# Optimization experiments

Hardware: AMD Instinct MI355X
Metric: run time of the kernel (lower is better)

## Reference

```python
import jax, jax.numpy as jnp
import numpy as np

D_MODEL = 256
N_HEADS = 8
HEAD_DIM = D_MODEL // N_HEADS  # 32
N_LEVELS = 4
N_POINTS = 4
LEVEL_SHAPES = [(100, 100), (50, 50), (25, 25), (13, 13)]
LEVEL_STARTS = [0] + list(np.cumsum([h * w for h, w in LEVEL_SHAPES]))[:-1]
LEN_IN = int(sum(h * w for h, w in LEVEL_SHAPES))  # 13294
BATCH = 2
LEN_Q = LEN_IN  # encoder self-attention


def _offset_bias():
    # faithful to MSDeformAttn._reset_parameters for sampling_offsets bias
    thetas = np.arange(N_HEADS, dtype=np.float32) * (2.0 * np.pi / N_HEADS)
    grid = np.stack([np.cos(thetas), np.sin(thetas)], -1)
    grid = grid / np.abs(grid).max(-1, keepdims=True)
    grid = np.tile(grid.reshape(N_HEADS, 1, 1, 2), (1, N_LEVELS, N_POINTS, 1))
    for i in range(N_POINTS):
        grid[:, :, i, :] *= i + 1
    return jnp.asarray(grid.reshape(-1), dtype=jnp.float32)


def setup_inputs() -> dict:
    key = jax.random.key(0)
    ks = jax.random.split(key, 10)
    s = 1.0 / np.sqrt(D_MODEL)
    inp = {
        "query": jax.random.normal(ks[0], (BATCH, LEN_Q, D_MODEL), jnp.float32),
        "reference_points": jax.random.uniform(ks[1], (BATCH, LEN_Q, N_LEVELS, 2), jnp.float32),
        "input_flatten": jax.random.normal(ks[2], (BATCH, LEN_IN, D_MODEL), jnp.float32),
        "input_spatial_shapes": jnp.asarray(LEVEL_SHAPES, dtype=jnp.int32),
        "W_value": jax.random.normal(ks[3], (D_MODEL, D_MODEL), jnp.float32) * s,
        "b_value": jnp.zeros((D_MODEL,), jnp.float32),
        "W_off": jax.random.normal(ks[4], (D_MODEL, N_HEADS * N_LEVELS * N_POINTS * 2), jnp.float32) * 0.01,
        "b_off": _offset_bias(),
        "W_attn": jax.random.normal(ks[5], (D_MODEL, N_HEADS * N_LEVELS * N_POINTS), jnp.float32) * 0.01,
        "b_attn": jnp.zeros((N_HEADS * N_LEVELS * N_POINTS,), jnp.float32),
        "W_out": jax.random.normal(ks[6], (D_MODEL, D_MODEL), jnp.float32) * s,
        "b_out": jnp.zeros((D_MODEL,), jnp.float32),
    }
    return inp


def _corner(v_t, ix, iy, h, w):
    # v_t: (n, M, h*w, D); ix/iy: (n, M, LqP) int32. Zero padding outside.
    valid = (ix >= 0) & (ix < w) & (iy >= 0) & (iy < h)
    idx = jnp.clip(iy, 0, h - 1) * w + jnp.clip(ix, 0, w - 1)
    g = jnp.take_along_axis(v_t, idx[..., None], axis=2)  # (n, M, LqP, D)
    return g * valid[..., None].astype(v_t.dtype)


def _ms_deform_attn(query, reference_points, input_flatten,
                    W_value, b_value, W_off, b_off, W_attn, b_attn, W_out, b_out):
    n, lq, _ = query.shape
    value = (input_flatten @ W_value + b_value).reshape(n, LEN_IN, N_HEADS, HEAD_DIM)
    offs = (query @ W_off + b_off).reshape(n, lq, N_HEADS, N_LEVELS, N_POINTS, 2)
    aw = jax.nn.softmax(
        (query @ W_attn + b_attn).reshape(n, lq, N_HEADS, N_LEVELS * N_POINTS), axis=-1
    ).reshape(n, lq, N_HEADS, N_LEVELS, N_POINTS)
    # offset_normalizer = (w, h) per level
    norm = jnp.asarray([[w, h] for h, w in LEVEL_SHAPES], dtype=query.dtype)
    loc = reference_points[:, :, None, :, None, :] + offs / norm[None, None, None, :, None, :]

    acc = jnp.zeros((n, N_HEADS, lq, HEAD_DIM), dtype=value.dtype)
    for l, (h, w) in enumerate(LEVEL_SHAPES):
        s0 = LEVEL_STARTS[l]
        v_t = jnp.transpose(value[:, s0:s0 + h * w], (0, 2, 1, 3))  # (n, M, hw, D)
        ll = loc[:, :, :, l]  # (n, lq, M, P, 2) in [0,1]
        # grid_sample bilinear, align_corners=False: pixel = coord*size - 0.5
        x = ll[..., 0] * w - 0.5
        y = ll[..., 1] * h - 0.5
        x0 = jnp.floor(x); y0 = jnp.floor(y)
        tx = x - x0; ty = y - y0
        ix0 = x0.astype(jnp.int32); iy0 = y0.astype(jnp.int32)
        flat = lambda a: jnp.transpose(a, (0, 2, 1, 3)).reshape(n, N_HEADS, lq * N_POINTS)
        ix0f, iy0f = flat(ix0), flat(iy0)
        txf = flat(tx)[..., None]; tyf = flat(ty)[..., None]
        g00 = _corner(v_t, ix0f, iy0f, h, w)
        g01 = _corner(v_t, ix0f + 1, iy0f, h, w)
        g10 = _corner(v_t, ix0f, iy0f + 1, h, w)
        g11 = _corner(v_t, ix0f + 1, iy0f + 1, h, w)
        samp = (g00 * (1 - txf) * (1 - tyf) + g01 * txf * (1 - tyf)
                + g10 * (1 - txf) * tyf + g11 * txf * tyf)
        samp = samp.reshape(n, N_HEADS, lq, N_POINTS, HEAD_DIM)
        wl = jnp.transpose(aw[:, :, :, l], (0, 2, 1, 3))[..., None]  # (n, M, lq, P, 1)
        acc = acc + (samp * wl).sum(axis=3)

    out = jnp.transpose(acc, (0, 2, 1, 3)).reshape(n, lq, D_MODEL)
    return out @ W_out + b_out


def reference(query, reference_points, input_flatten, input_spatial_shapes,
              W_value, b_value, W_off, b_off, W_attn, b_attn, W_out, b_out):
    # input_spatial_shapes carried for signature fidelity; level geometry is static.
    return _ms_deform_attn(query, reference_points, input_flatten,
                           W_value, b_value, W_off, b_off, W_attn, b_attn, W_out, b_out)
```

## Files before the change

### kernel.cpp

```cpp
#include <hip/hip_runtime.h>

#define NH 8
#define HD 32
#define NL 4
#define NP 4
#define DM 256
#define LEN_IN_C 13294
#define LQ_C 13294
#define B_C 2
#define M_TOTAL (B_C * LQ_C)
#define MT_TILES 1662

typedef __attribute__((ext_vector_type(8))) short short8;
typedef __attribute__((ext_vector_type(4))) float floatx4;

__device__ __forceinline__ unsigned short f2bf(float x) {
    union { float f; unsigned int u; } a; a.f = x;
    unsigned int r = (a.u + 0x7FFFu + ((a.u >> 16) & 1u)) >> 16;
    return (unsigned short)r;
}
__device__ __forceinline__ float bflo(unsigned int u) {
    union { unsigned int u; float f; } a; a.u = u << 16; return a.f;
}
__device__ __forceinline__ float bfhi(unsigned int u) {
    union { unsigned int u; float f; } a; a.u = u & 0xffff0000u; return a.f;
}

__global__ __launch_bounds__(256) void conv_a_kernel(const float* __restrict__ A0,
                                                     unsigned short* __restrict__ D0,
                                                     const float* __restrict__ A1,
                                                     unsigned short* __restrict__ D1,
                                                     int M) {
    const float* A = blockIdx.y ? A1 : A0;
    unsigned short* Asw = blockIdx.y ? D1 : D0;
    const int u = blockIdx.x * 256 + threadIdx.x;
    const int lane = u & 63;
    const int kc = (u >> 6) & 7;
    const int rt = u >> 9;
    const int row = rt * 16 + (lane & 15);
    const int col0 = kc * 32 + (lane >> 4) * 8;
    unsigned short tmp[8];
    if (row < M) {
        const float4 f0 = *(const float4*)(A + (size_t)row * 256 + col0);
        const float4 f1 = *(const float4*)(A + (size_t)row * 256 + col0 + 4);
        tmp[0] = f2bf(f0.x); tmp[1] = f2bf(f0.y); tmp[2] = f2bf(f0.z); tmp[3] = f2bf(f0.w);
        tmp[4] = f2bf(f1.x); tmp[5] = f2bf(f1.y); tmp[6] = f2bf(f1.z); tmp[7] = f2bf(f1.w);
    } else {
#pragma unroll
        for (int j = 0; j < 8; ++j) tmp[j] = 0;
    }
    short8 v;
#pragma unroll
    for (int j = 0; j < 8; ++j) v[j] = (short)tmp[j];
    ((short8*)Asw)[u] = v;
}

__device__ __forceinline__ void conv_b_body(const float* __restrict__ W,
                                            unsigned short* __restrict__ Bsw,
                                            int Nsrc, int NTsrc, int NTtotal, int ntOff,
                                            int vblk) {
    const int u = vblk * 256 + threadIdx.x;
    const int lane = u & 63;
    const int unit = u >> 6;
    const int ntl = unit % NTsrc;
    const int kc = unit / NTsrc;
    const int n = ntl * 16 + (lane & 15);
    const int k0 = kc * 32 + (lane >> 4) * 8;
    short8 v;
#pragma unroll
    for (int j = 0; j < 8; ++j)
        v[j] = (short)f2bf(W[(size_t)(k0 + j) * Nsrc + n]);
    ((short8*)Bsw)[(size_t)(kc * NTtotal + ntOff + ntl) * 64 + lane] = v;
}

__global__ __launch_bounds__(256) void conv_weights_kernel(const float* __restrict__ Wv,
                                                           const float* __restrict__ Woff,
                                                           const float* __restrict__ Wattn,
                                                           const float* __restrict__ Wout,
                                                           const float* __restrict__ boff,
                                                           const float* __restrict__ battn,
                                                           unsigned short* __restrict__ BswV,
                                                           unsigned short* __restrict__ BswOA,
                                                           unsigned short* __restrict__ BswO,
                                                           float* __restrict__ fbias) {
    const int blk = blockIdx.x;
    if (blk < 32)        conv_b_body(Wv,    BswV,  256, 16, 16, 0,  blk);
    else if (blk < 64)   conv_b_body(Woff,  BswOA, 256, 16, 24, 0,  blk - 32);
    else if (blk < 80)   conv_b_body(Wattn, BswOA, 128,  8, 24, 16, blk - 64);
    else if (blk < 112)  conv_b_body(Wout,  BswO,  256, 16, 16, 0,  blk - 80);
    else {
        const int t = (blk - 112) * 256 + threadIdx.x;
        if (t < 384) fbias[t] = (t < 256) ? boff[t] : battn[t - 256];
    }
}

template <int NT, bool OUT_BF16>
__global__ __launch_bounds__(256) void mfma_gemm_kernel(const unsigned short* __restrict__ Asw,
                                                        const unsigned short* __restrict__ Bsw,
                                                        const float* __restrict__ bias,
                                                        void* __restrict__ Cout, int M) {
    constexpr int NTW = NT / 4;
    const int tid = threadIdx.x;
    const int lane = tid & 63;
    const int wave = tid >> 6;
    const int rt0 = blockIdx.x * 2;

    const short8* Au = (const short8*)Asw;
    const short8* Bu = (const short8*)Bsw;

    floatx4 acc[2][NTW];
#pragma unroll
    for (int r = 0; r < 2; ++r)
#pragma unroll
        for (int t = 0; t < NTW; ++t) acc[r][t] = (floatx4){0.f, 0.f, 0.f, 0.f};

#pragma unroll 2
    for (int kc = 0; kc < 8; ++kc) {
        const short8 a0 = Au[(size_t)(rt0 * 8 + kc) * 64 + lane];
        const short8 a1 = Au[(size_t)((rt0 + 1) * 8 + kc) * 64 + lane];
#pragma unroll
        for (int t = 0; t < NTW; ++t) {
            const short8 b = Bu[(size_t)(kc * NT + wave * NTW + t) * 64 + lane];
            acc[0][t] = __builtin_amdgcn_mfma_f32_16x16x32_bf16(a0, b, acc[0][t], 0, 0, 0);
            acc[1][t] = __builtin_amdgcn_mfma_f32_16x16x32_bf16(a1, b, acc[1][t], 0, 0, 0);
        }
    }

    const int N = NT * 16;
    const int colq = lane & 15;
    const int rowq = (lane >> 4) * 4;
#pragma unroll
    for (int t = 0; t < NTW; ++t) {
        const int col = (wave * NTW + t) * 16 + colq;
        const float bc = bias[col];
#pragma unroll
        for (int r = 0; r < 2; ++r) {
            const int rowb = (rt0 + r) * 16 + rowq;
#pragma unroll
            for (int reg = 0; reg < 4; ++reg) {
                const int row = rowb + reg;
                if (row < M) {
                    const float v = acc[r][t][reg] + bc;
                    if (OUT_BF16)
                        ((unsigned short*)Cout)[(size_t)row * N + col] = f2bf(v);
                    else
                        ((float*)Cout)[(size_t)row * N + col] = v;
                }
            }
        }
    }
}

__global__ __launch_bounds__(256, 6) void msda_sample_kernel(const float* __restrict__ refp,
                                                             const unsigned short* __restrict__ value,
                                                             const float* __restrict__ fused,
                                                             unsigned short* __restrict__ AccSw) {
    constexpr int lvl_hw[4] = {100, 50, 25, 13};
    constexpr int lvl_s[4] = {0, 10000, 12500, 13125};

    const int bq0 = blockIdx.x * 4;
    const int tid = threadIdx.x;

    __shared__ float s_ref[32];
    __shared__ int4 s_pi[4 * 8 * 17];
    __shared__ float4 s_pw[4 * 8 * 17];

    if (tid < 32) s_ref[tid] = refp[(size_t)bq0 * 8 + tid];
    __syncthreads();

#pragma unroll
    for (int jj = 0; jj < 2; ++jj) {
        const int job = jj * 256 + tid;
        const int qq = job >> 7;
        const int t = job & 127;
        const int h = t >> 4;
        const int l = (t >> 2) & 3;
        const int bq = bq0 + qq;
        const int b = (bq >= LQ_C) ? 1 : 0;

        const float logit = fused[(size_t)bq * 384 + 256 + t];
        float m = logit;
#pragma unroll
        for (int mask = 1; mask < 16; mask <<= 1) m = fmaxf(m, __shfl_xor(m, mask));
        const float e = expf(logit - m);
        float s = e;
#pragma unroll
        for (int mask = 1; mask < 16; mask <<= 1) s += __shfl_xor(s, mask);
        const float aw = e / s;

        const int whl = lvl_hw[l];
        const float fwh = (float)whl;
        const float2 oxy = *(const float2*)(fused + (size_t)bq * 384 + t * 2);
        const float x = s_ref[qq * 8 + l * 2] * fwh + oxy.x - 0.5f;
        const float y = s_ref[qq * 8 + l * 2 + 1] * fwh + oxy.y - 0.5f;
        const float x0f = floorf(x), y0f = floorf(y);
        const float tx = x - x0f, ty = y - y0f;
        const int ix0 = (int)x0f, iy0 = (int)y0f;

        const bool xv0 = (unsigned)ix0 < (unsigned)whl;
        const bool xv1 = (unsigned)(ix0 + 1) < (unsigned)whl;
        const bool yv0 = (unsigned)iy0 < (unsigned)whl;
        const bool yv1 = (unsigned)(iy0 + 1) < (unsigned)whl;

        const int cx0 = min(max(ix0, 0), whl - 1);
        const int cx1 = min(max(ix0 + 1, 0), whl - 1);
        const int cy0 = min(max(iy0, 0), whl - 1);
        const int cy1 = min(max(iy0 + 1, 0), whl - 1);

        const int base = (b * LEN_IN_C + lvl_s[l]) * 256 + h * 32;
        const int r0 = base + cy0 * (whl * 256);
        const int r1 = base + cy1 * (whl * 256);
        int4 ii;
        ii.x = (r0 + cx0 * 256) * 2;
        ii.y = (r0 + cx1 * 256) * 2;
        ii.z = (r1 + cx0 * 256) * 2;
        ii.w = (r1 + cx1 * 256) * 2;
        float4 wv;
        wv.x = (xv0 && yv0) ? aw * (1.f - tx) * (1.f - ty) : 0.f;
        wv.y = (xv1 && yv0) ? aw * tx * (1.f - ty) : 0.f;
        wv.z = (xv0 && yv1) ? aw * (1.f - tx) * ty : 0.f;
        wv.w = (xv1 && yv1) ? aw * tx * ty : 0.f;
        const int slot = (qq * 8 + h) * 17 + (t & 15);
        s_pi[slot] = ii;
        s_pw[slot] = wv;
    }
    __syncthreads();

    const int qq = tid >> 6;
    const int h = (tid >> 3) & 7;
    const int l8 = tid & 7;
    const int d4 = l8 * 8;
    const char* vb = (const char*)value;
    const int pbase = (qq * 8 + h) * 17;

    float4 acc0 = {0.f, 0.f, 0.f, 0.f};
    float4 acc1 = {0.f, 0.f, 0.f, 0.f};
#pragma unroll 2
    for (int pt = 0; pt < 16; ++pt) {
        const int4 ii = s_pi[pbase + pt];
        const float4 wv = s_pw[pbase + pt];
        const uint2 v00 = *(const uint2*)(vb + (ii.x + d4));
        const uint2 v01 = *(const uint2*)(vb + (ii.y + d4));
        const uint2 v10 = *(const uint2*)(vb + (ii.z + d4));
        const uint2 v11 = *(const uint2*)(vb + (ii.w + d4));
        acc0.x += wv.x * bflo(v00.x); acc0.y += wv.x * bfhi(v00.x);
        acc0.z += wv.x * bflo(v00.y); acc0.w += wv.x * bfhi(v00.y);
        acc1.x += wv.y * bflo(v01.x); acc1.y += wv.y * bfhi(v01.x);
        acc1.z += wv.y * bflo(v01.y); acc1.w += wv.y * bfhi(v01.y);
        acc0.x += wv.z * bflo(v10.x); acc0.y += wv.z * bfhi(v10.x);
        acc0.z += wv.z * bflo(v10.y); acc0.w += wv.z * bfhi(v10.y);
        acc1.x += wv.w * bflo(v11.x); acc1.y += wv.w * bfhi(v11.x);
        acc1.z += wv.w * bflo(v11.y); acc1.w += wv.w * bfhi(v11.y);
    }
    const float4 acc = {acc0.x + acc1.x, acc0.y + acc1.y, acc0.z + acc1.z, acc0.w + acc1.w};

    const int bq = bq0 + qq;
    const int rt = bq >> 4, mm = bq & 15;
    const int col = h * 32 + l8 * 4;
    const int kc = col >> 5, q2 = (col >> 3) & 3, j = col & 7;
    unsigned int p0 = (unsigned int)f2bf(acc.x) | ((unsigned int)f2bf(acc.y) << 16);
    unsigned int p1 = (unsigned int)f2bf(acc.z) | ((unsigned int)f2bf(acc.w) << 16);
    uint2 pk; pk.x = p0; pk.y = p1;
    *(uint2*)(AccSw + ((size_t)((rt * 8 + kc) * 64 + (q2 * 16 + mm)) * 8 + j)) = pk;
}

extern "C" void kernel_launch(void* const* d_in, const int* in_sizes, int n_in,
                              void* d_out, int out_size, void* d_ws, size_t ws_size,
                              hipStream_t stream) {
    const float* query  = (const float*)d_in[0];
    const float* refp   = (const float*)d_in[1];
    const float* inflat = (const float*)d_in[2];
    const float* Wv    = (const float*)d_in[4];
    const float* bv    = (const float*)d_in[5];
    const float* Woff  = (const float*)d_in[6];
    const float* boff  = (const float*)d_in[7];
    const float* Wattn = (const float*)d_in[8];
    const float* battn = (const float*)d_in[9];
    const float* Wout  = (const float*)d_in[10];
    const float* bout  = (const float*)d_in[11];
    float* out = (float*)d_out;

    char* p = (char*)d_ws;
    const size_t aswBytes = (size_t)MT_TILES * 8 * 64 * 8 * sizeof(unsigned short);
    unsigned short* AswQ = (unsigned short*)p;           p += aswBytes;
    unsigned short* AswS = (unsigned short*)p;           p += aswBytes;
    unsigned short* BswV = (unsigned short*)p;           p += (size_t)8 * 16 * 64 * 8 * 2;
    unsigned short* BswOA = (unsigned short*)p;          p += (size_t)8 * 24 * 64 * 8 * 2;
    unsigned short* BswO = (unsigned short*)p;           p += (size_t)8 * 16 * 64 * 8 * 2;
    float* fbias = (float*)p;                            p += 384 * sizeof(float);
    unsigned short* value = (unsigned short*)p;          p += (size_t)M_TOTAL * 256 * 2;
    float* fused = (float*)p;                            p += (size_t)M_TOTAL * 384 * 4;

    const int M = M_TOTAL;

    conv_weights_kernel<<<114, 256, 0, stream>>>(Wv, Woff, Wattn, Wout, boff, battn,
                                                 BswV, BswOA, BswO, fbias);
    conv_a_kernel<<<dim3(MT_TILES * 2, 2), 256, 0, stream>>>(inflat, AswS, query, AswQ, M);

    const int gemmBlocks = MT_TILES / 2;
    mfma_gemm_kernel<16, true><<<gemmBlocks, 256, 0, stream>>>(AswS, BswV, bv, value, M);
    mfma_gemm_kernel<24, false><<<gemmBlocks, 256, 0, stream>>>(AswQ, BswOA, fbias, fused, M);
    msda_sample_kernel<<<M / 4, 256, 0, stream>>>(refp, value, fused, AswS);
    mfma_gemm_kernel<16, false><<<gemmBlocks, 256, 0, stream>>>(AswS, BswO, bout, out, M);
}
```

Measured before the change: 230.8 us.

## Fuse fp32-to-bf16 input conversion into GEMMs and merge value/offset GEMMs

Removes the separate conv_a kernel. The value and offset/attention GEMMs now read fp32 rows directly and pack them to bf16 with byte-permute rounding, and both projections run in one launch. The GEMM now covers one row tile per block, with register double-buffering of the A and B fragments. The sampling kernel batches its gathers four points at a time to raise memory-level parallelism, and its occupancy hint is lowered. The cost is that the B fragments are no longer shared across two row tiles. The new rounding also drops round-to-nearest-even tie handling.

```diff
diff --git a/kernel.cpp b/kernel.cpp
--- a/kernel.cpp
+++ b/kernel.cpp
@@ -26,33 +26,21 @@
     union { unsigned int u; float f; } a; a.u = u & 0xffff0000u; return a.f;
 }
 
-__global__ __launch_bounds__(256) void conv_a_kernel(const float* __restrict__ A0,
-                                                     unsigned short* __restrict__ D0,
-                                                     const float* __restrict__ A1,
-                                                     unsigned short* __restrict__ D1,
-                                                     int M) {
-    const float* A = blockIdx.y ? A1 : A0;
-    unsigned short* Asw = blockIdx.y ? D1 : D0;
-    const int u = blockIdx.x * 256 + threadIdx.x;
-    const int lane = u & 63;
-    const int kc = (u >> 6) & 7;
-    const int rt = u >> 9;
-    const int row = rt * 16 + (lane & 15);
-    const int col0 = kc * 32 + (lane >> 4) * 8;
-    unsigned short tmp[8];
-    if (row < M) {
-        const float4 f0 = *(const float4*)(A + (size_t)row * 256 + col0);
-        const float4 f1 = *(const float4*)(A + (size_t)row * 256 + col0 + 4);
-        tmp[0] = f2bf(f0.x); tmp[1] = f2bf(f0.y); tmp[2] = f2bf(f0.z); tmp[3] = f2bf(f0.w);
-        tmp[4] = f2bf(f1.x); tmp[5] = f2bf(f1.y); tmp[6] = f2bf(f1.z); tmp[7] = f2bf(f1.w);
-    } else {
-#pragma unroll
-        for (int j = 0; j < 8; ++j) tmp[j] = 0;
-    }
-    short8 v;
-#pragma unroll
-    for (int j = 0; j < 8; ++j) v[j] = (short)tmp[j];
-    ((short8*)Asw)[u] = v;
+__device__ __forceinline__ short8 pack_bf16_8(float4 f0, float4 f1) {
+    const unsigned a0 = __float_as_uint(f0.x) + 0x8000u;
+    const unsigned a1 = __float_as_uint(f0.y) + 0x8000u;
+    const unsigned a2 = __float_as_uint(f0.z) + 0x8000u;
+    const unsigned a3 = __float_as_uint(f0.w) + 0x8000u;
+    const unsigned b0 = __float_as_uint(f1.x) + 0x8000u;
+    const unsigned b1 = __float_as_uint(f1.y) + 0x8000u;
+    const unsigned b2 = __float_as_uint(f1.z) + 0x8000u;
+    const unsigned b3 = __float_as_uint(f1.w) + 0x8000u;
+    union { unsigned u[4]; short8 s; } r;
+    r.u[0] = __builtin_amdgcn_perm(a1, a0, 0x07060302);
+    r.u[1] = __builtin_amdgcn_perm(a3, a2, 0x07060302);
+    r.u[2] = __builtin_amdgcn_perm(b1, b0, 0x07060302);
+    r.u[3] = __builtin_amdgcn_perm(b3, b2, 0x07060302);
+    return r.s;
 }
 
 __device__ __forceinline__ void conv_b_body(const float* __restrict__ W,
@@ -94,35 +82,61 @@
     }
 }
 
-template <int NT, bool OUT_BF16>
-__global__ __launch_bounds__(256) void mfma_gemm_kernel(const unsigned short* __restrict__ Asw,
-                                                        const unsigned short* __restrict__ Bsw,
-                                                        const float* __restrict__ bias,
-                                                        void* __restrict__ Cout, int M) {
+template <int NT, bool OUT_BF16, bool A_F32>
+__device__ __forceinline__ void gemm_body(const void* __restrict__ Aptr,
+                                          const short8* __restrict__ Bu,
+                                          const float* __restrict__ bias,
+                                          void* __restrict__ Cout, int M, int rt) {
     constexpr int NTW = NT / 4;
     const int tid = threadIdx.x;
     const int lane = tid & 63;
     const int wave = tid >> 6;
-    const int rt0 = blockIdx.x * 2;
-
-    const short8* Au = (const short8*)Asw;
-    const short8* Bu = (const short8*)Bsw;
-
-    floatx4 acc[2][NTW];
-#pragma unroll
-    for (int r = 0; r < 2; ++r)
-#pragma unroll
-        for (int t = 0; t < NTW; ++t) acc[r][t] = (floatx4){0.f, 0.f, 0.f, 0.f};
-
-#pragma unroll 2
+
+    const int m = lane & 15;
+    const int q = lane >> 4;
+    int arow = rt * 16 + m; if (arow >= M) arow = M - 1;
+    const float* ap = (const float*)Aptr + (size_t)arow * 256 + q * 8;
+    const short8* Au = (const short8*)Aptr;
+
+    floatx4 acc[NTW];
+#pragma unroll
+    for (int t = 0; t < NTW; ++t) acc[t] = (floatx4){0.f, 0.f, 0.f, 0.f};
+
+    short8 a_cur, a_nxt;
+    short8 b_cur[NTW], b_nxt[NTW];
+
+    if (A_F32) {
+        const float4 f0 = *(const float4*)(ap);
+        const float4 f1 = *(const float4*)(ap + 4);
+        a_cur = pack_bf16_8(f0, f1);
+    } else {
+        a_cur = Au[(size_t)(rt * 8 + 0) * 64 + lane];
+    }
+#pragma unroll
+    for (int t = 0; t < NTW; ++t)
+        b_cur[t] = Bu[(size_t)(wave * NTW + t) * 64 + lane];
+
+#pragma unroll
     for (int kc = 0; kc < 8; ++kc) {
-        const short8 a0 = Au[(size_t)(rt0 * 8 + kc) * 64 + lane];
-        const short8 a1 = Au[(size_t)((rt0 + 1) * 8 + kc) * 64 + lane];
-#pragma unroll
-        for (int t = 0; t < NTW; ++t) {
-            const short8 b = Bu[(size_t)(kc * NT + wave * NTW + t) * 64 + lane];
-            acc[0][t] = __builtin_amdgcn_mfma_f32_16x16x32_bf16(a0, b, acc[0][t], 0, 0, 0);
-            acc[1][t] = __builtin_amdgcn_mfma_f32_16x16x32_bf16(a1, b, acc[1][t], 0, 0, 0);
+        if (kc < 7) {
+            if (A_F32) {
+                const float4 f0 = *(const float4*)(ap + (kc + 1) * 32);
+                const float4 f1 = *(const float4*)(ap + (kc + 1) * 32 + 4);
+                a_nxt = pack_bf16_8(f0, f1);
+            } else {
+                a_nxt = Au[(size_t)(rt * 8 + kc + 1) * 64 + lane];
+            }
+#pragma unroll
+            for (int t = 0; t < NTW; ++t)
+                b_nxt[t] = Bu[(size_t)((kc + 1) * NT + wave * NTW + t) * 64 + lane];
+        }
+#pragma unroll
+        for (int t = 0; t < NTW; ++t)
+            acc[t] = __builtin_amdgcn_mfma_f32_16x16x32_bf16(a_cur, b_cur[t], acc[t], 0, 0, 0);
+        if (kc < 7) {
+            a_cur = a_nxt;
+#pragma unroll
+            for (int t = 0; t < NTW; ++t) b_cur[t] = b_nxt[t];
         }
     }
 
@@ -134,24 +148,41 @@
         const int col = (wave * NTW + t) * 16 + colq;
         const float bc = bias[col];
 #pragma unroll
-        for (int r = 0; r < 2; ++r) {
-            const int rowb = (rt0 + r) * 16 + rowq;
-#pragma unroll
-            for (int reg = 0; reg < 4; ++reg) {
-                const int row = rowb + reg;
-                if (row < M) {
-                    const float v = acc[r][t][reg] + bc;
-                    if (OUT_BF16)
-                        ((unsigned short*)Cout)[(size_t)row * N + col] = f2bf(v);
-                    else
-                        ((float*)Cout)[(size_t)row * N + col] = v;
-                }
+        for (int reg = 0; reg < 4; ++reg) {
+            const int row = rt * 16 + rowq + reg;
+            if (row < M) {
+                const float v = acc[t][reg] + bc;
+                if (OUT_BF16)
+                    ((unsigned short*)Cout)[(size_t)row * N + col] = f2bf(v);
+                else
+                    ((float*)Cout)[(size_t)row * N + col] = v;
             }
         }
     }
 }
 
-__global__ __launch_bounds__(256, 6) void msda_sample_kernel(const float* __restrict__ refp,
+__global__ __launch_bounds__(256, 4) void dual_gemm_kernel(const float* __restrict__ inflat,
+                                                           const float* __restrict__ query,
+                                                           const short8* __restrict__ BuV,
+                                                           const short8* __restrict__ BuOA,
+                                                           const float* __restrict__ bv,
+                                                           const float* __restrict__ fbias,
+                                                           unsigned short* __restrict__ value,
+                                                           float* __restrict__ fused, int M) {
+    if (blockIdx.x < MT_TILES)
+        gemm_body<16, true, true>(inflat, BuV, bv, value, M, blockIdx.x);
+    else
+        gemm_body<24, false, true>(query, BuOA, fbias, fused, M, blockIdx.x - MT_TILES);
+}
+
+__global__ __launch_bounds__(256, 4) void out_gemm_kernel(const unsigned short* __restrict__ AccSw,
+                                                          const short8* __restrict__ BuO,
+                                                          const float* __restrict__ bout,
+                                                          float* __restrict__ out, int M) {
+    gemm_body<16, false, false>(AccSw, BuO, bout, out, M, blockIdx.x);
+}
+
+__global__ __launch_bounds__(256, 4) void msda_sample_kernel(const float* __restrict__ refp,
                                                              const unsigned short* __restrict__ value,
                                                              const float* __restrict__ fused,
                                                              unsigned short* __restrict__ AccSw) {
@@ -179,10 +210,10 @@
         const int b = (bq >= LQ_C) ? 1 : 0;
 
         const float logit = fused[(size_t)bq * 384 + 256 + t];
-        float m = logit;
-#pragma unroll
-        for (int mask = 1; mask < 16; mask <<= 1) m = fmaxf(m, __shfl_xor(m, mask));
-        const float e = expf(logit - m);
+        float mx = logit;
+#pragma unroll
+        for (int mask = 1; mask < 16; mask <<= 1) mx = fmaxf(mx, __shfl_xor(mx, mask));
+        const float e = expf(logit - mx);
         float s = e;
 #pragma unroll
         for (int mask = 1; mask < 16; mask <<= 1) s += __shfl_xor(s, mask);
@@ -229,28 +260,40 @@
     const int qq = tid >> 6;
     const int h = (tid >> 3) & 7;
     const int l8 = tid & 7;
-    const int d4 = l8 * 8;
-    const char* vb = (const char*)value;
+    const char* vbp = (const char*)value + l8 * 8;
     const int pbase = (qq * 8 + h) * 17;
 
     float4 acc0 = {0.f, 0.f, 0.f, 0.f};
     float4 acc1 = {0.f, 0.f, 0.f, 0.f};
-#pragma unroll 2
-    for (int pt = 0; pt < 16; ++pt) {
-        const int4 ii = s_pi[pbase + pt];
-        const float4 wv = s_pw[pbase + pt];
-        const uint2 v00 = *(const uint2*)(vb + (ii.x + d4));
-        const uint2 v01 = *(const uint2*)(vb + (ii.y + d4));
-        const uint2 v10 = *(const uint2*)(vb + (ii.z + d4));
-        const uint2 v11 = *(const uint2*)(vb + (ii.w + d4));
-        acc0.x += wv.x * bflo(v00.x); acc0.y += wv.x * bfhi(v00.x);
-        acc0.z += wv.x * bflo(v00.y); acc0.w += wv.x * bfhi(v00.y);
-        acc1.x += wv.y * bflo(v01.x); acc1.y += wv.y * bfhi(v01.x);
-        acc1.z += wv.y * bflo(v01.y); acc1.w += wv.y * bfhi(v01.y);
-        acc0.x += wv.z * bflo(v10.x); acc0.y += wv.z * bfhi(v10.x);
-        acc0.z += wv.z * bflo(v10.y); acc0.w += wv.z * bfhi(v10.y);
-        acc1.x += wv.w * bflo(v11.x); acc1.y += wv.w * bfhi(v11.x);
-        acc1.z += wv.w * bflo(v11.y); acc1.w += wv.w * bfhi(v11.y);
+#pragma unroll
+    for (int g = 0; g < 4; ++g) {
+        int4 ii[4]; float4 ww[4]; uint2 v[16];
+#pragma unroll
+        for (int p = 0; p < 4; ++p) {
+            ii[p] = s_pi[pbase + g * 4 + p];
+            ww[p] = s_pw[pbase + g * 4 + p];
+        }
+#pragma unroll
+        for (int p = 0; p < 4; ++p) {
+            v[p * 4 + 0] = *(const uint2*)(vbp + ii[p].x);
+            v[p * 4 + 1] = *(const uint2*)(vbp + ii[p].y);
+            v[p * 4 + 2] = *(const uint2*)(vbp + ii[p].z);
+            v[p * 4 + 3] = *(const uint2*)(vbp + ii[p].w);
+        }
+#pragma unroll
+        for (int p = 0; p < 4; ++p) {
+            const float4 wv = ww[p];
+            const uint2 v00 = v[p * 4 + 0], v01 = v[p * 4 + 1];
+            const uint2 v10 = v[p * 4 + 2], v11 = v[p * 4 + 3];
+            acc0.x += wv.x * bflo(v00.x); acc0.y += wv.x * bfhi(v00.x);
+            acc0.z += wv.x * bflo(v00.y); acc0.w += wv.x * bfhi(v00.y);
+            acc1.x += wv.y * bflo(v01.x); acc1.y += wv.y * bfhi(v01.x);
+            acc1.z += wv.y * bflo(v01.y); acc1.w += wv.y * bfhi(v01.y);
+            acc0.x += wv.z * bflo(v10.x); acc0.y += wv.z * bfhi(v10.x);
+            acc0.z += wv.z * bflo(v10.y); acc0.w += wv.z * bfhi(v10.y);
+            acc1.x += wv.w * bflo(v11.x); acc1.y += wv.w * bfhi(v11.x);
+            acc1.z += wv.w * bflo(v11.y); acc1.w += wv.w * bfhi(v11.y);
+        }
     }
     const float4 acc = {acc0.x + acc1.x, acc0.y + acc1.y, acc0.z + acc1.z, acc0.w + acc1.w};
 
@@ -282,8 +325,7 @@
 
     char* p = (char*)d_ws;
     const size_t aswBytes = (size_t)MT_TILES * 8 * 64 * 8 * sizeof(unsigned short);
-    unsigned short* AswQ = (unsigned short*)p;           p += aswBytes;
-    unsigned short* AswS = (unsigned short*)p;           p += aswBytes;
+    unsigned short* AccSw = (unsigned short*)p;          p += aswBytes;
     unsigned short* BswV = (unsigned short*)p;           p += (size_t)8 * 16 * 64 * 8 * 2;
     unsigned short* BswOA = (unsigned short*)p;          p += (size_t)8 * 24 * 64 * 8 * 2;
     unsigned short* BswO = (unsigned short*)p;           p += (size_t)8 * 16 * 64 * 8 * 2;
@@ -295,11 +337,9 @@
 
     conv_weights_kernel<<<114, 256, 0, stream>>>(Wv, Woff, Wattn, Wout, boff, battn,
                                                  BswV, BswOA, BswO, fbias);
-    conv_a_kernel<<<dim3(MT_TILES * 2, 2), 256, 0, stream>>>(inflat, AswS, query, AswQ, M);
-
-    const int gemmBlocks = MT_TILES / 2;
-    mfma_gemm_kernel<16, true><<<gemmBlocks, 256, 0, stream>>>(AswS, BswV, bv, value, M);
-    mfma_gemm_kernel<24, false><<<gemmBlocks, 256, 0, stream>>>(AswQ, BswOA, fbias, fused, M);
-    msda_sample_kernel<<<M / 4, 256, 0, stream>>>(refp, value, fused, AswS);
-    mfma_gemm_kernel<16, false><<<gemmBlocks, 256, 0, stream>>>(AswS, BswO, bout, out, M);
-}
+    dual_gemm_kernel<<<MT_TILES * 2, 256, 0, stream>>>(inflat, query,
+                                                       (const short8*)BswV, (const short8*)BswOA,
+                                                       bv, fbias, value, fused, M);
+    msda_sample_kernel<<<M / 4, 256, 0, stream>>>(refp, value, fused, AccSw);
+    out_gemm_kernel<<<MT_TILES, 256, 0, stream>>>(AccSw, (const short8*)BswO, bout, out, M);
+}
```

After: 250.4 us. +8.5%, slower.
